# Kernel tuning notes

Measured on AMD Instinct MI355X. Metric: run time of the kernel, lower is better.

## Reference

```python
import jax, jax.numpy as jnp
import numpy as np

N = 20000      # nodes
E = 320000     # edges
IN = 128       # in_channels
HID = 64       # hidden_channels (per-head out dim, concat=False -> mean over heads)
HEADS = 4
NEG_SLOPE = 0.2


def setup_inputs() -> dict:
    key = jax.random.key(0)
    ks = jax.random.split(key, 18)
    g = lambda i, shape: jax.random.normal(ks[i], shape, dtype=jnp.float32) * 0.05
    return {
        "x": jax.random.normal(ks[0], (N, IN), dtype=jnp.float32),
        "edge_index": jax.random.randint(ks[1], (2, E), 0, N),
        # GATConv params: lin weight (no bias in PyG lin), att_src/att_dst, out bias
        "W0": g(2, (IN, HEADS * HID)),
        "W1": g(3, (HID, HEADS * HID)),
        "W2": g(4, (HID, HEADS * HID)),
        "W3": g(5, (HID, HEADS * HID)),
        "a_src": g(6, (4, HEADS, HID)),
        "a_dst": g(7, (4, HEADS, HID)),
        "gat_b": g(8, (4, HID)),
        # residual projection for layer 0 (in_channels != hidden_channels)
        "res_W": g(9, (IN, HID)),
        "res_b": g(10, (HID,)),
        # edge classifier MLP: 2*HID -> HID -> HID -> 1
        "lin_W0": g(11, (2 * HID, HID)),
        "lin_b0": g(12, (HID,)),
        "lin_W1": g(13, (HID, HID)),
        "lin_b1": g(14, (HID,)),
        "lin_W2": g(15, (HID, 1)),
        "lin_b2": g(16, (1,)),
    }


def gat_conv(x, src, dst, W, asrc, adst, b, n):
    # x: [n, F_in]; src/dst: [E_tot] (self-loops included); W: [F_in, H*C]
    h = (x @ W).reshape(n, HEADS, HID)                     # [n, H, C]
    s_src = (h * asrc).sum(-1)                             # [n, H]
    s_dst = (h * adst).sum(-1)                             # [n, H]
    e = jax.nn.leaky_relu(s_src[src] + s_dst[dst], NEG_SLOPE)  # [E_tot, H]
    # segment softmax over incoming edges of each dst node
    m = jax.ops.segment_max(e, dst, num_segments=n)        # [n, H]
    p = jnp.exp(e - m[dst])
    z = jax.ops.segment_sum(p, dst, num_segments=n)
    alpha = p / z[dst]                                     # [E_tot, H]
    out = jax.ops.segment_sum(alpha[:, :, None] * h[src], dst, num_segments=n)  # [n, H, C]
    return out.mean(axis=1) + b                            # concat=False -> mean over heads


def reference(x, edge_index, W0, W1, W2, W3, a_src, a_dst, gat_b,
              res_W, res_b, lin_W0, lin_b0, lin_W1, lin_b1, lin_W2, lin_b2):
    n = x.shape[0]
    loop = jnp.arange(n)
    src = jnp.concatenate([edge_index[0], loop])  # PyG GATConv adds self-loops
    dst = jnp.concatenate([edge_index[1], loop])
    Ws = [W0, W1, W2, W3]
    h = x
    for i in range(4):
        h_prev = h
        h = gat_conv(h, src, dst, Ws[i], a_src[i], a_dst[i], gat_b[i], n)
        if i == 0:
            h = h + h_prev @ res_W + res_b   # projected residual
        else:
            h = h + h_prev
        h = jax.nn.elu(h)
    row, col = edge_index[0], edge_index[1]
    er = jnp.concatenate([h[row], h[col]], axis=1)        # [E, 2*HID]
    er = jax.nn.relu(er @ lin_W0 + lin_b0)                # shapes differ -> no residual
    er = jax.nn.relu(er @ lin_W1 + lin_b1 + er)           # shapes match -> residual
    logits = er @ lin_W2 + lin_b2                          # [E, 1]
    return logits
```

## Files before the change

### kernel.cpp

```cpp
#include <hip/hip_runtime.h>
#include <hip/hip_bf16.h>

#define NSLOPE 0.2f

typedef short bf16x8 __attribute__((ext_vector_type(8)));
typedef float f32x4 __attribute__((ext_vector_type(4)));

__device__ __forceinline__ unsigned short f2b(float f) {
    unsigned u = __float_as_uint(f);
    unsigned r = (u + 0x7FFFu + ((u >> 16) & 1u)) >> 16;
    return (unsigned short)r;
}
__device__ __forceinline__ float b2f_lo(unsigned w) {
    return __uint_as_float(w << 16);
}
__device__ __forceinline__ float b2f_hi(unsigned w) {
    return __uint_as_float(w & 0xFFFF0000u);
}
__device__ __forceinline__ float b2f_s(short s) {
    return __uint_as_float(((unsigned)(unsigned short)s) << 16);
}


__global__ __launch_bounds__(256) void hist_deg(const int* __restrict__ ei,
                                                int* __restrict__ deg, int E,
                                                int n) {
    int t = blockIdx.x * 256 + threadIdx.x;
    int Etot = E + n;
    if (t >= Etot) return;
    int d = (t < E) ? ei[E + t] : (t - E);
    atomicAdd(&deg[d], 1);
}

__global__ __launch_bounds__(256) void scan_blk(const int* __restrict__ deg,
                                                int* __restrict__ local,
                                                int* __restrict__ bsum, int n) {
    __shared__ int sm[256];
    const int base = blockIdx.x * 1024;
    const int t = threadIdx.x;
    const int i0 = base + t * 4;
    int v0 = 0, v1 = 0, v2 = 0, v3 = 0;
    if (i0 + 3 < n) {
        int4 v = *(const int4*)(deg + i0);
        v0 = v.x; v1 = v.y; v2 = v.z; v3 = v.w;
    } else {
        if (i0 < n) v0 = deg[i0];
        if (i0 + 1 < n) v1 = deg[i0 + 1];
        if (i0 + 2 < n) v2 = deg[i0 + 2];
    }
    int s = v0 + v1 + v2 + v3;
    sm[t] = s;
    __syncthreads();
    for (int off = 1; off < 256; off <<= 1) {
        int val = (t >= off) ? sm[t - off] : 0;
        __syncthreads();
        sm[t] += val;
        __syncthreads();
    }
    int ex = sm[t] - s;
    if (t == 255) bsum[blockIdx.x] = sm[255];
    if (i0 < n) local[i0] = ex;
    if (i0 + 1 < n) local[i0 + 1] = ex + v0;
    if (i0 + 2 < n) local[i0 + 2] = ex + v0 + v1;
    if (i0 + 3 < n) local[i0 + 3] = ex + v0 + v1 + v2;
}

__global__ __launch_bounds__(256) void scan_top(const int* __restrict__ bsum,
                                                int* __restrict__ boff,
                                                int nb) {
    __shared__ int sm[256];
    const int t = threadIdx.x;
    int s = (t < nb) ? bsum[t] : 0;
    sm[t] = s;
    __syncthreads();
    for (int off = 1; off < 256; off <<= 1) {
        int val = (t >= off) ? sm[t - off] : 0;
        __syncthreads();
        sm[t] += val;
        __syncthreads();
    }
    if (t < nb) boff[t] = sm[t] - s;
}

__global__ __launch_bounds__(256) void scan_add(const int* __restrict__ local,
                                                const int* __restrict__ boff,
                                                int* __restrict__ rowstart,
                                                int* __restrict__ cursor,
                                                int n, int Etot) {
    int i = blockIdx.x * 256 + threadIdx.x;
    if (i > n) return;
    if (i == n) {
        rowstart[n] = Etot;
        return;
    }
    int v = local[i] + boff[i >> 10];
    rowstart[i] = v;
    cursor[i] = v;
}

__global__ __launch_bounds__(256) void fill_csr(const int* __restrict__ ei,
                                                int* __restrict__ cursor,
                                                int* __restrict__ csr, int E,
                                                int n) {
    int t = blockIdx.x * 256 + threadIdx.x;
    int Etot = E + n;
    if (t >= Etot) return;
    int s, d;
    if (t < E) { s = ei[t]; d = ei[E + t]; } else { s = d = t - E; }
    int pos = atomicAdd(&cursor[d], 1);
    csr[pos] = s;
}

__global__ __launch_bounds__(256) void prep_weights(
    const float* __restrict__ W0, const float* __restrict__ W1,
    const float* __restrict__ W2, const float* __restrict__ W3,
    const float* __restrict__ resW, const float* __restrict__ linW0,
    const float* __restrict__ linW1, short* __restrict__ Wt0,
    short* __restrict__ Wt1, short* __restrict__ Wt2, short* __restrict__ Wt3,
    short* __restrict__ WtR, short* __restrict__ WtU, short* __restrict__ WtV,
    short* __restrict__ WbT) {
    const float* src;
    short* dst;
    int K, NC, rowoff = 0;
    switch (blockIdx.x) {
        case 0: src = W0; dst = Wt0; K = 128; NC = 256; break;
        case 1: src = W1; dst = Wt1; K = 64; NC = 256; break;
        case 2: src = W2; dst = Wt2; K = 64; NC = 256; break;
        case 3: src = W3; dst = Wt3; K = 64; NC = 256; break;
        case 4: src = resW; dst = WtR; K = 128; NC = 64; break;
        case 5: src = linW0; dst = WtU; K = 64; NC = 64; break;
        case 6: src = linW0; dst = WtV; K = 64; NC = 64; rowoff = 64; break;
        default: src = linW1; dst = WbT; K = 64; NC = 64; break;
    }
    for (int idx = blockIdx.y * 256 + threadIdx.x; idx < K * NC;
         idx += 256 * 16) {
        int k = idx / NC, nn = idx - k * NC;
        dst[nn * K + k] = (short)f2b(src[(k + rowoff) * NC + nn]);
    }
}

__global__ __launch_bounds__(128) void bias_prep(const float* __restrict__ b0,
                                                 float* __restrict__ b128) {
    int i = threadIdx.x;
    b128[i] = (i < 64) ? b0[i] : 0.f;
}

__global__ __launch_bounds__(256) void convert_x(const float* __restrict__ x,
                                                 short* __restrict__ xb,
                                                 int total) {
    int idx = (blockIdx.x * 256 + threadIdx.x) * 4;
    if (idx >= total) return;
    float4 v = *(const float4*)(x + idx);
    ushort4 o;
    o.x = f2b(v.x); o.y = f2b(v.y); o.z = f2b(v.z); o.w = f2b(v.w);
    *(ushort4*)(xb + idx) = o;
}

template <int K, int NG, int OM>
__global__ __launch_bounds__(256) void mfma_gemm(
    const short* __restrict__ Xb, const short* __restrict__ Wt,
    const float* __restrict__ bias, uint2* __restrict__ Hq,
    const float* __restrict__ as_l, const float* __restrict__ ad_l,
    float* __restrict__ Ssrc, float* __restrict__ Sdst,
    float* __restrict__ OutF, short* __restrict__ OutB, int n) {
    constexpr int XSTR = K + 8;
    constexpr int NC = NG * 16;
    __shared__ __align__(16) short Xs[64 * XSTR];
    __shared__ __align__(16) short Ws[NC * 40];
    const int tid = threadIdx.x;
    const int nb = blockIdx.x * 64;
    constexpr int CH = K / 8;
    for (int idx = tid; idx < 64 * CH; idx += 256) {
        int row = idx / CH, c = idx - row * CH;
        uint4 v = make_uint4(0, 0, 0, 0);
        if (nb + row < n)
            v = *(const uint4*)(Xb + (size_t)(nb + row) * K + c * 8);
        *(uint4*)(Xs + row * XSTR + c * 8) = v;
    }
    const int wid = tid >> 6;
    const int lane = tid & 63;
    const int t = lane & 15, quad = lane >> 4;
    f32x4 acc[NG];
#pragma unroll
    for (int g = 0; g < NG; ++g) acc[g] = (f32x4){0.f, 0.f, 0.f, 0.f};
#pragma unroll 1
    for (int kc = 0; kc < K / 32; ++kc) {
        __syncthreads();
        for (int idx = tid; idx < NC * 4; idx += 256) {
            int row = idx >> 2, c = idx & 3;
            uint4 v = *(const uint4*)(Wt + (size_t)row * K + kc * 32 + c * 8);
            *(uint4*)(Ws + row * 40 + c * 8) = v;
        }
        __syncthreads();
        bf16x8 a =
            *(const bf16x8*)(Xs + (wid * 16 + t) * XSTR + kc * 32 + quad * 8);
#pragma unroll
        for (int g = 0; g < NG; ++g) {
            bf16x8 b = *(const bf16x8*)(Ws + (g * 16 + t) * 40 + quad * 8);
            acc[g] = __builtin_amdgcn_mfma_f32_16x16x32_bf16(a, b, acc[g], 0, 0, 0);
        }
    }
    if (OM == 1) {
#pragma unroll
        for (int r = 0; r < 4; ++r) {
            int node = nb + wid * 16 + quad * 4 + r;
            if (node >= n) continue;
#pragma unroll
            for (int g = 0; g < 4; ++g) {
                unsigned p01 = ((unsigned)f2b(acc[g + 4][r]) << 16) |
                               (unsigned)f2b(acc[g][r]);
                unsigned p23 = ((unsigned)f2b(acc[g + 12][r]) << 16) |
                               (unsigned)f2b(acc[g + 8][r]);
                Hq[(size_t)node * 64 + g * 16 + t] = make_uint2(p01, p23);
            }
        }
        float asv[16], adv[16];
#pragma unroll
        for (int G = 0; G < 16; ++G) {
            asv[G] = as_l[G * 16 + t];
            adv[G] = ad_l[G * 16 + t];
        }
#pragma unroll
        for (int r = 0; r < 4; ++r) {
            int node = nb + wid * 16 + quad * 4 + r;
            float pv[8];
#pragma unroll
            for (int h = 0; h < 4; ++h) {
                float ps = 0.f, pd = 0.f;
#pragma unroll
                for (int j = 0; j < 4; ++j) {
                    float a = acc[h * 4 + j][r];
                    ps += a * asv[h * 4 + j];
                    pd += a * adv[h * 4 + j];
                }
                pv[h] = ps;
                pv[4 + h] = pd;
            }
#pragma unroll
            for (int off = 1; off < 16; off <<= 1) {
#pragma unroll
                for (int i = 0; i < 8; ++i) pv[i] += __shfl_xor(pv[i], off, 64);
            }
            if (t == 0 && node < n) {
                *(float4*)&Ssrc[node * 4] =
                    make_float4(pv[0], pv[1], pv[2], pv[3]);
                *(float4*)&Sdst[node * 4] =
                    make_float4(pv[4], pv[5], pv[6], pv[7]);
            }
        }
    } else {
        float bv[NG];
#pragma unroll
        for (int g = 0; g < NG; ++g) bv[g] = bias ? bias[g * 16 + t] : 0.f;
#pragma unroll
        for (int r = 0; r < 4; ++r) {
            int node = nb + wid * 16 + quad * 4 + r;
            if (node >= n) continue;
            if (OM == 0) {
#pragma unroll
                for (int g = 0; g < NG; ++g)
                    OutF[(size_t)node * NC + g * 16 + t] = acc[g][r] + bv[g];
            } else {
#pragma unroll
                for (int g = 0; g < NG; ++g)
                    OutB[(size_t)node * NC + g * 16 + t] =
                        (short)f2b(acc[g][r] + bv[g]);
            }
        }
    }
}

__global__ __launch_bounds__(256) void gat_gather(
    const int* __restrict__ csr, const int* __restrict__ rowstart,
    const float* __restrict__ Ssrc, const float* __restrict__ Sdst,
    const uint2* __restrict__ Hq, const float* __restrict__ gb,
    const float* __restrict__ resid, float* __restrict__ featOut,
    short* __restrict__ featB, int n) {
    const int wid = threadIdx.x >> 6;
    const int lane = threadIdx.x & 63;
    const int node = blockIdx.x * 4 + wid;
    if (node >= n) return;
    const int start = rowstart[node];
    const int end = rowstart[node + 1];
    const int el = lane >> 2;
    const int h = lane & 3;
    const float4 sd = *(const float4*)&Sdst[node * 4];
    const float sdh = (h == 0) ? sd.x : (h == 1) ? sd.y : (h == 2) ? sd.z : sd.w;

    float u0 = 0.f, u1 = 0.f, u2 = 0.f, u3 = 0.f, zacc = 0.f;
    for (int b = start; b < end; b += 16) {
        const int nEd = min(16, end - b);
        int s = 0;
        float p = 0.f;
        if (el < nEd) {
            s = csr[b + el];
            float sc = Ssrc[s * 4 + h] + sdh;
            sc = sc > 0.f ? sc : NSLOPE * sc;
            p = __expf(sc);
        }
        zacc += p;
        if (nEd == 16) {
#pragma unroll 4
            for (int j = 0; j < 16; ++j) {
                int sj = __shfl(s, j * 4, 64);
                float p0 = __shfl(p, j * 4 + 0, 64);
                float p1 = __shfl(p, j * 4 + 1, 64);
                float p2 = __shfl(p, j * 4 + 2, 64);
                float p3 = __shfl(p, j * 4 + 3, 64);
                uint2 hv = Hq[(size_t)sj * 64 + lane];
                u0 += p0 * b2f_lo(hv.x);
                u1 += p1 * b2f_hi(hv.x);
                u2 += p2 * b2f_lo(hv.y);
                u3 += p3 * b2f_hi(hv.y);
            }
        } else {
#pragma unroll 4
            for (int j = 0; j < nEd; ++j) {
                int sj = __shfl(s, j * 4, 64);
                float p0 = __shfl(p, j * 4 + 0, 64);
                float p1 = __shfl(p, j * 4 + 1, 64);
                float p2 = __shfl(p, j * 4 + 2, 64);
                float p3 = __shfl(p, j * 4 + 3, 64);
                uint2 hv = Hq[(size_t)sj * 64 + lane];
                u0 += p0 * b2f_lo(hv.x);
                u1 += p1 * b2f_hi(hv.x);
                u2 += p2 * b2f_lo(hv.y);
                u3 += p3 * b2f_hi(hv.y);
            }
        }
    }
#pragma unroll
    for (int off = 4; off < 64; off <<= 1) zacc += __shfl_xor(zacc, off, 64);
    const float z0 = __shfl(zacc, 0, 64);
    const float z1 = __shfl(zacc, 1, 64);
    const float z2 = __shfl(zacc, 2, 64);
    const float z3 = __shfl(zacc, 3, 64);
    float val = 0.25f * (u0 / z0 + u1 / z1 + u2 / z2 + u3 / z3) + gb[lane] +
                resid[(size_t)node * 64 + lane];
    val = val > 0.f ? val : expm1f(val);
    featOut[(size_t)node * 64 + lane] = val;
    featB[(size_t)node * 64 + lane] = (short)f2b(val);
}

__global__ __launch_bounds__(256) void edge_mlp3(
    const int* __restrict__ ei, const unsigned* __restrict__ UV,
    const short* __restrict__ WbT, const float* __restrict__ bb,
    const float* __restrict__ Wc, const float* __restrict__ bc,
    float* __restrict__ out, int E) {
    __shared__ __align__(16) short t1b[64 * 72];
    __shared__ __align__(16) short wbs[64 * 72];
    const int tid = threadIdx.x;
    const int eBase = blockIdx.x * 64;
    for (int idx = tid; idx < 512; idx += 256) {
        int row = idx >> 3, c = idx & 7;
        *(uint4*)(wbs + row * 72 + c * 8) =
            *(const uint4*)(WbT + row * 64 + c * 8);
    }
    {
        const int j = tid & 31;
        const int eg = tid >> 5;
        int rr[8], cc[8];
#pragma unroll
        for (int it = 0; it < 8; ++it) {
            int e = eBase + it * 8 + eg;
            rr[it] = (e < E) ? ei[e] : 0;
            cc[it] = (e < E) ? ei[E + e] : 0;
        }
#pragma unroll
        for (int it = 0; it < 8; ++it) {
            unsigned uu = UV[(size_t)rr[it] * 64 + j];
            unsigned vv = UV[(size_t)cc[it] * 64 + 32 + j];
            float lo = fmaxf(b2f_lo(uu) + b2f_lo(vv), 0.f);
            float hi = fmaxf(b2f_hi(uu) + b2f_hi(vv), 0.f);
            *(unsigned*)(t1b + (it * 8 + eg) * 72 + j * 2) =
                ((unsigned)f2b(hi) << 16) | (unsigned)f2b(lo);
        }
    }
    __syncthreads();
    const int w = tid >> 6, lane = tid & 63;
    const int t = lane & 15, quad = lane >> 4;
    f32x4 acc[4];
#pragma unroll
    for (int g = 0; g < 4; ++g) acc[g] = (f32x4){0.f, 0.f, 0.f, 0.f};
#pragma unroll
    for (int kc = 0; kc < 2; ++kc) {
        bf16x8 a = *(const bf16x8*)(t1b + (w * 16 + t) * 72 + kc * 32 + quad * 8);
#pragma unroll
        for (int g = 0; g < 4; ++g) {
            bf16x8 b = *(const bf16x8*)(wbs + (g * 16 + t) * 72 + kc * 32 + quad * 8);
            acc[g] = __builtin_amdgcn_mfma_f32_16x16x32_bf16(a, b, acc[g], 0, 0, 0);
        }
    }
    float wcv[4], bbv[4];
#pragma unroll
    for (int g = 0; g < 4; ++g) {
        wcv[g] = Wc[g * 16 + t];
        bbv[g] = bb[g * 16 + t];
    }
    const float bcv = bc[0];
#pragma unroll
    for (int r = 0; r < 4; ++r) {
        int el = w * 16 + quad * 4 + r;
        float part = 0.f;
#pragma unroll
        for (int g = 0; g < 4; ++g) {
            float t1v = b2f_s(t1b[el * 72 + g * 16 + t]);
            float t2 = fmaxf(acc[g][r] + bbv[g] + t1v, 0.f);
            part += t2 * wcv[g];
        }
        part += __shfl_xor(part, 1, 64);
        part += __shfl_xor(part, 2, 64);
        part += __shfl_xor(part, 4, 64);
        part += __shfl_xor(part, 8, 64);
        int e = eBase + el;
        if (t == 0 && e < E) out[e] = part + bcv;
    }
}

extern "C" void kernel_launch(void* const* d_in, const int* in_sizes, int n_in,
                              void* d_out, int out_size, void* d_ws,
                              size_t ws_size, hipStream_t stream) {
    const float* x = (const float*)d_in[0];
    const int* ei = (const int*)d_in[1];
    const float* W0 = (const float*)d_in[2];
    const float* W1 = (const float*)d_in[3];
    const float* W2 = (const float*)d_in[4];
    const float* W3 = (const float*)d_in[5];
    const float* a_src = (const float*)d_in[6];
    const float* a_dst = (const float*)d_in[7];
    const float* gat_b = (const float*)d_in[8];
    const float* res_W = (const float*)d_in[9];
    const float* res_b = (const float*)d_in[10];
    const float* lin_W0 = (const float*)d_in[11];
    const float* lin_b0 = (const float*)d_in[12];
    const float* lin_W1 = (const float*)d_in[13];
    const float* lin_b1 = (const float*)d_in[14];
    const float* lin_W2 = (const float*)d_in[15];
    const float* lin_b2 = (const float*)d_in[16];
    float* out = (float*)d_out;

    const int N = in_sizes[0] / 128;
    const int E = in_sizes[1] / 2;
    const int Etot = E + N;

    float* ws = (float*)d_ws;
    uint2* Hq = (uint2*)ws;
    float* feat = (float*)(Hq + (size_t)N * 64);
    float* res = feat + (size_t)N * 64;
    short* xb = (short*)(res + (size_t)N * 64);
    short* featb = xb;
    float* Ssrc = (float*)(xb + (size_t)N * 128);
    float* Sdst = Ssrc + (size_t)N * 4;
    short* Wt0 = (short*)(Sdst + (size_t)N * 4);
    short* Wt1 = Wt0 + 256 * 128;
    short* Wt2 = Wt1 + 256 * 64;
    short* Wt3 = Wt2 + 256 * 64;
    short* WtR = Wt3 + 256 * 64;
    short* WtU = WtR + 64 * 128;
    short* WtV = WtU + 64 * 64;
    short* WbT = WtV + 64 * 64;
    int* deg = (int*)(WbT + 64 * 64);
    int* rowstart = deg + N;
    int* cursor = rowstart + N + 1;
    int* csr = cursor + N;
    int* locals = csr + Etot;
    int* bsum = locals + N;
    int* boff = bsum + 256;
    float* bias128 = (float*)(boff + 256);
    short* UVb = (short*)Hq;

    const int gemmBlocks = (N + 63) / 64;
    const int edgeBlocks = (Etot + 255) / 256;
    const int nodeW = (N + 3) / 4;
    const int scanBlocks = (N + 1023) / 1024;
    const short* Wts[4] = {Wt0, Wt1, Wt2, Wt3};

    hipMemsetAsync(deg, 0, (size_t)N * sizeof(int), stream);
    hist_deg<<<edgeBlocks, 256, 0, stream>>>(ei, deg, E, N);
    scan_blk<<<scanBlocks, 256, 0, stream>>>(deg, locals, bsum, N);
    scan_top<<<1, 256, 0, stream>>>(bsum, boff, scanBlocks);
    scan_add<<<(N + 256) / 256, 256, 0, stream>>>(locals, boff, rowstart,
                                                  cursor, N, Etot);
    fill_csr<<<edgeBlocks, 256, 0, stream>>>(ei, cursor, csr, E, N);

    prep_weights<<<dim3(8, 16), 256, 0, stream>>>(W0, W1, W2, W3, res_W,
                                                  lin_W0, lin_W1, Wt0, Wt1,
                                                  Wt2, Wt3, WtR, WtU, WtV, WbT);
    bias_prep<<<1, 128, 0, stream>>>(lin_b0, bias128);
    convert_x<<<(N * 128 / 4 + 255) / 256, 256, 0, stream>>>(x, xb, N * 128);

    for (int i = 0; i < 4; ++i) {
        if (i == 0)
            mfma_gemm<128, 16, 1><<<gemmBlocks, 256, 0, stream>>>(
                xb, Wt0, nullptr, Hq, a_src, a_dst, Ssrc, Sdst, nullptr,
                nullptr, N);
        else
            mfma_gemm<64, 16, 1><<<gemmBlocks, 256, 0, stream>>>(
                featb, Wts[i], nullptr, Hq, a_src + i * 256, a_dst + i * 256,
                Ssrc, Sdst, nullptr, nullptr, N);
        if (i == 0)
            mfma_gemm<128, 4, 0><<<gemmBlocks, 256, 0, stream>>>(
                xb, WtR, res_b, nullptr, nullptr, nullptr, nullptr, nullptr,
                res, nullptr, N);
        const float* resid = (i == 0) ? res : feat;
        gat_gather<<<nodeW, 256, 0, stream>>>(csr, rowstart, Ssrc, Sdst, Hq,
                                              gat_b + i * 64, resid, feat,
                                              featb, N);
    }

    mfma_gemm<64, 8, 2><<<gemmBlocks, 256, 0, stream>>>(
        featb, WtU, bias128, nullptr, nullptr, nullptr, nullptr, nullptr,
        nullptr, UVb, N);
    edge_mlp3<<<(E + 63) / 64, 256, 0, stream>>>(
        ei, (const unsigned*)UVb, WbT, lin_b1, lin_W2, lin_b2, out, E);
}
```

Baseline: 357.0 us.

## Precompute per-edge attention exponentials in a separate edge kernel before gather

Moves the leaky-relu and exp attention score computation out of the per-node gather into a new edge-parallel kernel that writes float4 weights per CSR edge. The CSR now stores (src,dst) pairs so the edge kernel can read both endpoints. The gather becomes a simple serial loop over edges with wave-uniform bounds, with no shuffles. The bias prep kernel is also folded into prep_weights to save a launch. In exchange, each layer adds an extra kernel launch and writes then rereads 16 bytes per edge, and the CSR entries double in size.

```diff
diff --git a/kernel.cpp b/kernel.cpp
--- a/kernel.cpp
+++ b/kernel.cpp
@@ -100,7 +100,7 @@
 
 __global__ __launch_bounds__(256) void fill_csr(const int* __restrict__ ei,
                                                 int* __restrict__ cursor,
-                                                int* __restrict__ csr, int E,
+                                                int2* __restrict__ csr2, int E,
                                                 int n) {
     int t = blockIdx.x * 256 + threadIdx.x;
     int Etot = E + n;
@@ -108,17 +108,18 @@
     int s, d;
     if (t < E) { s = ei[t]; d = ei[E + t]; } else { s = d = t - E; }
     int pos = atomicAdd(&cursor[d], 1);
-    csr[pos] = s;
+    csr2[pos] = make_int2(s, d);
 }
 
 __global__ __launch_bounds__(256) void prep_weights(
     const float* __restrict__ W0, const float* __restrict__ W1,
     const float* __restrict__ W2, const float* __restrict__ W3,
     const float* __restrict__ resW, const float* __restrict__ linW0,
-    const float* __restrict__ linW1, short* __restrict__ Wt0,
-    short* __restrict__ Wt1, short* __restrict__ Wt2, short* __restrict__ Wt3,
-    short* __restrict__ WtR, short* __restrict__ WtU, short* __restrict__ WtV,
-    short* __restrict__ WbT) {
+    const float* __restrict__ linW1, const float* __restrict__ linB0,
+    short* __restrict__ Wt0, short* __restrict__ Wt1, short* __restrict__ Wt2,
+    short* __restrict__ Wt3, short* __restrict__ WtR, short* __restrict__ WtU,
+    short* __restrict__ WtV, short* __restrict__ WbT,
+    float* __restrict__ bias128) {
     const float* src;
     short* dst;
     int K, NC, rowoff = 0;
@@ -130,19 +131,19 @@
         case 4: src = resW; dst = WtR; K = 128; NC = 64; break;
         case 5: src = linW0; dst = WtU; K = 64; NC = 64; break;
         case 6: src = linW0; dst = WtV; K = 64; NC = 64; rowoff = 64; break;
-        default: src = linW1; dst = WbT; K = 64; NC = 64; break;
+        case 7: src = linW1; dst = WbT; K = 64; NC = 64; break;
+        default: {
+            if (blockIdx.y == 0 && threadIdx.x < 128)
+                bias128[threadIdx.x] =
+                    (threadIdx.x < 64) ? linB0[threadIdx.x] : 0.f;
+            return;
+        }
     }
     for (int idx = blockIdx.y * 256 + threadIdx.x; idx < K * NC;
          idx += 256 * 16) {
         int k = idx / NC, nn = idx - k * NC;
         dst[nn * K + k] = (short)f2b(src[(k + rowoff) * NC + nn]);
     }
-}
-
-__global__ __launch_bounds__(128) void bias_prep(const float* __restrict__ b0,
-                                                 float* __restrict__ b128) {
-    int i = threadIdx.x;
-    b128[i] = (i < 64) ? b0[i] : 0.f;
 }
 
 __global__ __launch_bounds__(256) void convert_x(const float* __restrict__ x,
@@ -270,71 +271,47 @@
     }
 }
 
+__global__ __launch_bounds__(256) void edge_scores(
+    const int2* __restrict__ csr2, const float* __restrict__ Ssrc,
+    const float* __restrict__ Sdst, float4* __restrict__ p4, int Etot) {
+    int e = blockIdx.x * 256 + threadIdx.x;
+    if (e >= Etot) return;
+    int2 sd = csr2[e];
+    float4 ss = *(const float4*)&Ssrc[sd.x * 4];
+    float4 dd = *(const float4*)&Sdst[sd.y * 4];
+    float c0 = ss.x + dd.x, c1 = ss.y + dd.y, c2 = ss.z + dd.z,
+          c3 = ss.w + dd.w;
+    c0 = c0 > 0.f ? c0 : NSLOPE * c0;
+    c1 = c1 > 0.f ? c1 : NSLOPE * c1;
+    c2 = c2 > 0.f ? c2 : NSLOPE * c2;
+    c3 = c3 > 0.f ? c3 : NSLOPE * c3;
+    p4[e] = make_float4(__expf(c0), __expf(c1), __expf(c2), __expf(c3));
+}
+
 __global__ __launch_bounds__(256) void gat_gather(
-    const int* __restrict__ csr, const int* __restrict__ rowstart,
-    const float* __restrict__ Ssrc, const float* __restrict__ Sdst,
-    const uint2* __restrict__ Hq, const float* __restrict__ gb,
-    const float* __restrict__ resid, float* __restrict__ featOut,
-    short* __restrict__ featB, int n) {
+    const int2* __restrict__ csr2, const int* __restrict__ rowstart,
+    const float4* __restrict__ p4, const uint2* __restrict__ Hq,
+    const float* __restrict__ gb, const float* __restrict__ resid,
+    float* __restrict__ featOut, short* __restrict__ featB, int n) {
     const int wid = threadIdx.x >> 6;
     const int lane = threadIdx.x & 63;
     const int node = blockIdx.x * 4 + wid;
     if (node >= n) return;
-    const int start = rowstart[node];
-    const int end = rowstart[node + 1];
-    const int el = lane >> 2;
-    const int h = lane & 3;
-    const float4 sd = *(const float4*)&Sdst[node * 4];
-    const float sdh = (h == 0) ? sd.x : (h == 1) ? sd.y : (h == 2) ? sd.z : sd.w;
-
-    float u0 = 0.f, u1 = 0.f, u2 = 0.f, u3 = 0.f, zacc = 0.f;
-    for (int b = start; b < end; b += 16) {
-        const int nEd = min(16, end - b);
-        int s = 0;
-        float p = 0.f;
-        if (el < nEd) {
-            s = csr[b + el];
-            float sc = Ssrc[s * 4 + h] + sdh;
-            sc = sc > 0.f ? sc : NSLOPE * sc;
-            p = __expf(sc);
-        }
-        zacc += p;
-        if (nEd == 16) {
+    const int start = __builtin_amdgcn_readfirstlane(rowstart[node]);
+    const int end = __builtin_amdgcn_readfirstlane(rowstart[node + 1]);
+    float u0 = 0.f, u1 = 0.f, u2 = 0.f, u3 = 0.f;
+    float z0 = 0.f, z1 = 0.f, z2 = 0.f, z3 = 0.f;
 #pragma unroll 4
-            for (int j = 0; j < 16; ++j) {
-                int sj = __shfl(s, j * 4, 64);
-                float p0 = __shfl(p, j * 4 + 0, 64);
-                float p1 = __shfl(p, j * 4 + 1, 64);
-                float p2 = __shfl(p, j * 4 + 2, 64);
-                float p3 = __shfl(p, j * 4 + 3, 64);
-                uint2 hv = Hq[(size_t)sj * 64 + lane];
-                u0 += p0 * b2f_lo(hv.x);
-                u1 += p1 * b2f_hi(hv.x);
-                u2 += p2 * b2f_lo(hv.y);
-                u3 += p3 * b2f_hi(hv.y);
-            }
-        } else {
-#pragma unroll 4
-            for (int j = 0; j < nEd; ++j) {
-                int sj = __shfl(s, j * 4, 64);
-                float p0 = __shfl(p, j * 4 + 0, 64);
-                float p1 = __shfl(p, j * 4 + 1, 64);
-                float p2 = __shfl(p, j * 4 + 2, 64);
-                float p3 = __shfl(p, j * 4 + 3, 64);
-                uint2 hv = Hq[(size_t)sj * 64 + lane];
-                u0 += p0 * b2f_lo(hv.x);
-                u1 += p1 * b2f_hi(hv.x);
-                u2 += p2 * b2f_lo(hv.y);
-                u3 += p3 * b2f_hi(hv.y);
-            }
-        }
-    }
-#pragma unroll
-    for (int off = 4; off < 64; off <<= 1) zacc += __shfl_xor(zacc, off, 64);
-    const float z0 = __shfl(zacc, 0, 64);
-    const float z1 = __shfl(zacc, 1, 64);
-    const float z2 = __shfl(zacc, 2, 64);
-    const float z3 = __shfl(zacc, 3, 64);
+    for (int e = start; e < end; ++e) {
+        int sj = csr2[e].x;
+        float4 p = p4[e];
+        uint2 hv = Hq[(size_t)sj * 64 + lane];
+        u0 += p.x * b2f_lo(hv.x);
+        u1 += p.y * b2f_hi(hv.x);
+        u2 += p.z * b2f_lo(hv.y);
+        u3 += p.w * b2f_hi(hv.y);
+        z0 += p.x; z1 += p.y; z2 += p.z; z3 += p.w;
+    }
     float val = 0.25f * (u0 / z0 + u1 / z1 + u2 / z2 + u3 / z3) + gb[lane] +
                 resid[(size_t)node * 64 + lane];
     val = val > 0.f ? val : expm1f(val);
@@ -462,11 +439,12 @@
     int* deg = (int*)(WbT + 64 * 64);
     int* rowstart = deg + N;
     int* cursor = rowstart + N + 1;
-    int* csr = cursor + N;
-    int* locals = csr + Etot;
+    int* locals = cursor + N;
     int* bsum = locals + N;
     int* boff = bsum + 256;
     float* bias128 = (float*)(boff + 256);
+    int2* csr2 = (int2*)(((size_t)(bias128 + 128) + 15) & ~(size_t)15);
+    float4* p4 = (float4*)(((size_t)(csr2 + Etot) + 15) & ~(size_t)15);
     short* UVb = (short*)Hq;
 
     const int gemmBlocks = (N + 63) / 64;
@@ -481,12 +459,11 @@
     scan_top<<<1, 256, 0, stream>>>(bsum, boff, scanBlocks);
     scan_add<<<(N + 256) / 256, 256, 0, stream>>>(locals, boff, rowstart,
                                                   cursor, N, Etot);
-    fill_csr<<<edgeBlocks, 256, 0, stream>>>(ei, cursor, csr, E, N);
-
-    prep_weights<<<dim3(8, 16), 256, 0, stream>>>(W0, W1, W2, W3, res_W,
-                                                  lin_W0, lin_W1, Wt0, Wt1,
-                                                  Wt2, Wt3, WtR, WtU, WtV, WbT);
-    bias_prep<<<1, 128, 0, stream>>>(lin_b0, bias128);
+    fill_csr<<<edgeBlocks, 256, 0, stream>>>(ei, cursor, csr2, E, N);
+
+    prep_weights<<<dim3(9, 16), 256, 0, stream>>>(
+        W0, W1, W2, W3, res_W, lin_W0, lin_W1, lin_b0, Wt0, Wt1, Wt2, Wt3,
+        WtR, WtU, WtV, WbT, bias128);
     convert_x<<<(N * 128 / 4 + 255) / 256, 256, 0, stream>>>(x, xb, N * 128);
 
     for (int i = 0; i < 4; ++i) {
@@ -498,12 +475,14 @@
             mfma_gemm<64, 16, 1><<<gemmBlocks, 256, 0, stream>>>(
                 featb, Wts[i], nullptr, Hq, a_src + i * 256, a_dst + i * 256,
                 Ssrc, Sdst, nullptr, nullptr, N);
+        edge_scores<<<edgeBlocks, 256, 0, stream>>>(csr2, Ssrc, Sdst, p4,
+                                                    Etot);
         if (i == 0)
             mfma_gemm<128, 4, 0><<<gemmBlocks, 256, 0, stream>>>(
                 xb, WtR, res_b, nullptr, nullptr, nullptr, nullptr, nullptr,
                 res, nullptr, N);
         const float* resid = (i == 0) ? res : feat;
-        gat_gather<<<nodeW, 256, 0, stream>>>(csr, rowstart, Ssrc, Sdst, Hq,
+        gat_gather<<<nodeW, 256, 0, stream>>>(csr2, rowstart, p4, Hq,
                                               gat_b + i * 64, resid, feat,
                                               featb, N);
     }
```

Measured after the change: 353.3 us. Within noise of the previous version (-1.0%).
